# Kernel tuning notes

Hardware: AMD Instinct MI355X
Metric: run time of the kernel (lower is better)

Reference implementation:

```python
import jax, jax.numpy as jnp
import numpy as np

N, E, D = 50000, 600000, 128  # nodes, edges, units (== vert_dim, so no W_adapt)


def glorot(key, shape):
    lim = np.sqrt(6.0 / (shape[0] + shape[1]))
    return jax.random.uniform(key, shape, jnp.float32, -lim, lim)


def setup_inputs() -> dict:
    key = jax.random.key(0)
    ks = jax.random.split(key, 8)
    X = jax.random.normal(ks[0], (N, D), jnp.float32)
    ref_a = jax.random.randint(ks[1], (E,), 0, N, jnp.int32)
    ref_b = jax.random.randint(ks[2], (E,), 0, N, jnp.int32)
    # msg_net: two Dense(D) layers, inner_activation=None (linear)
    W1 = glorot(ks[3], (D, D)); b1 = jnp.zeros((D,), jnp.float32)
    W2 = glorot(ks[4], (D, D)); b2 = jnp.zeros((D,), jnp.float32)
    # keras GRUCell (reset_after=True): kernel [D,3D], recurrent_kernel [D,3D], bias [2,3D]
    gru_kernel = glorot(ks[5], (D, 3 * D))
    gru_rkernel = glorot(ks[6], (D, 3 * D))
    gru_bias = jnp.zeros((2, 3 * D), jnp.float32)
    return {"X": X, "ref_a": ref_a, "ref_b": ref_b,
            "W1": W1, "b1": b1, "W2": W2, "b2": b2,
            "gru_kernel": gru_kernel, "gru_rkernel": gru_rkernel, "gru_bias": gru_bias}


def _ggnn(X, ref_a, ref_b, W1, b1, W2, b2, gru_kernel, gru_rkernel, gru_bias):
    # msg_net (depth=2, linear inner activation)
    X_msg = (X @ W1 + b1) @ W2 + b2                       # [N, D]
    # wl1_convolution, undirected: scatter-add both directions
    agg = jnp.zeros_like(X_msg)
    agg = agg.at[ref_b].add(X_msg[ref_a])                 # a -> b
    agg = agg.at[ref_a].add(X_msg[ref_b])                 # b -> a (directed=False)
    # keras GRUCell update: inputs = agg, state = X  (reset_after=True)
    mx = agg @ gru_kernel + gru_bias[0]                   # [N, 3D]
    mh = X @ gru_rkernel + gru_bias[1]                    # [N, 3D]
    xz, xr, xh = jnp.split(mx, 3, axis=-1)
    rz, rr, rh = jnp.split(mh, 3, axis=-1)
    z = jax.nn.sigmoid(xz + rz)
    r = jax.nn.sigmoid(xr + rr)
    hh = jnp.tanh(xh + r * rh)
    return z * X + (1.0 - z) * hh                         # [N, D]


def reference(X, ref_a, ref_b, W1, b1, W2, b2, gru_kernel, gru_rkernel, gru_bias):
    return _ggnn(X, ref_a, ref_b, W1, b1, W2, b2, gru_kernel, gru_rkernel, gru_bias)
```

## Files before the change

### kernel.cpp

```cpp
#include <hip/hip_runtime.h>
#include <cstdint>
#include <cstddef>

typedef __bf16 bf16x8 __attribute__((ext_vector_type(8)));
typedef float  f32x4  __attribute__((ext_vector_type(4)));
typedef short  s16x8  __attribute__((ext_vector_type(8)));

static __device__ __forceinline__ float bf2f(short s) {
    union { unsigned u; float f; } v;
    v.u = ((unsigned)(unsigned short)s) << 16;
    return v.f;
}
static __device__ __forceinline__ short f2bf(float f) {
    unsigned u = __float_as_uint(f);
    u += 0x7fffu + ((u >> 16) & 1u);
    return (short)(u >> 16);
}
static __device__ __forceinline__ float sigmoid_(float x) {
    return 1.0f / (1.0f + __expf(-x));
}
static __device__ __forceinline__ float tanh_(float x) {
    float ax = fabsf(x);
    float e  = __expf(-2.0f * ax);
    float t  = (1.0f - e) / (1.0f + e);
    return copysignf(t, x);
}

#define MFMA(a, b, c) __builtin_amdgcn_mfma_f32_16x16x32_bf16((a), (b), (c), 0, 0, 0)

static __device__ __forceinline__ int lidx8(int r, int ch) {
    return r * 128 + ((ch ^ (r & 15)) << 3);
}
static __device__ __forceinline__ int lidx(int r, int col) {
    return r * 128 + ((((col >> 3) ^ (r & 15)) << 3) | (col & 7));
}

#define BLOCKS1     256
#define STRIPE_CAP  64
#define BUCKET_REG  (BLOCKS1 * STRIPE_CAP)
#define NODE_CAP    96
#define SENTINEL    0xFFFFFFFFu

__global__ __launch_bounds__(256) void transpose_kernel(
    const float* __restrict__ W1, const float* __restrict__ W2,
    const float* __restrict__ GK, const float* __restrict__ GR,
    short* __restrict__ W1t, short* __restrict__ W2t,
    short* __restrict__ GKt, short* __restrict__ GRt)
{
    int i = blockIdx.x * 256 + threadIdx.x;
    if (i < 16384) {
        int k = i >> 7, n = i & 127;
        W1t[n * 128 + k] = f2bf(W1[i]);
        W2t[n * 128 + k] = f2bf(W2[i]);
    }
    if (i < 49152) {
        int k = i / 384, n = i - k * 384;
        GKt[n * 128 + k] = f2bf(GK[i]);
        GRt[n * 128 + k] = f2bf(GR[i]);
    }
}

static __device__ __forceinline__ s16x8 cvt8(const float* p) {
    f32x4 a0 = *(const f32x4*)(p);
    f32x4 a1 = *(const f32x4*)(p + 4);
    s16x8 v;
    v[0] = f2bf(a0[0]); v[1] = f2bf(a0[1]); v[2] = f2bf(a0[2]); v[3] = f2bf(a0[3]);
    v[4] = f2bf(a1[0]); v[5] = f2bf(a1[1]); v[6] = f2bf(a1[2]); v[7] = f2bf(a1[3]);
    return v;
}

__global__ __launch_bounds__(512) void msg_kernel(
    const float* __restrict__ X, const short* __restrict__ W1t,
    const float* __restrict__ b1, const short* __restrict__ W2t,
    const float* __restrict__ b2, short* __restrict__ msg, int N)
{
    __shared__ short ldsA[128 * 128];
    __shared__ short ldsW[128 * 128];
    const int tid  = threadIdx.x;
    const int m0   = blockIdx.x * 128;
    const int lane = tid & 63, wv = tid >> 6;
    const int q = lane >> 4, c = lane & 15;
    const int rowA0 = wv * 16;

    for (int i = tid; i < 128 * 16; i += 512) {
        int r = i >> 4, ch = i & 15;
        s16x8 v;
        if (m0 + r < N) v = cvt8(X + (size_t)(m0 + r) * 128 + ch * 8);
        else            v = (s16x8)0;
        *(s16x8*)(ldsA + lidx8(r, ch)) = v;
        *(s16x8*)(ldsW + lidx8(r, ch)) = *(const s16x8*)(W1t + r * 128 + ch * 8);
    }
    __syncthreads();

    f32x4 acc[8];
#pragma unroll
    for (int n = 0; n < 8; n++) acc[n] = (f32x4)0.0f;

#pragma unroll
    for (int ks = 0; ks < 4; ks++) {
        int kc = ks * 4 + q;
        bf16x8 a0 = __builtin_bit_cast(bf16x8, *(const s16x8*)(ldsA + lidx8(rowA0 + c, kc)));
#pragma unroll
        for (int n = 0; n < 8; n++) {
            bf16x8 b = __builtin_bit_cast(bf16x8, *(const s16x8*)(ldsW + lidx8(n * 16 + c, kc)));
            acc[n] = MFMA(a0, b, acc[n]);
        }
    }

#pragma unroll
    for (int n = 0; n < 8; n++) {
        float bias = b1[n * 16 + c];
#pragma unroll
        for (int i = 0; i < 4; i++) {
            int row = rowA0 + q * 4 + i;
            ldsA[lidx(row, n * 16 + c)] = f2bf(acc[n][i] + bias);
        }
    }
    __syncthreads();
    for (int i = tid; i < 128 * 16; i += 512) {
        int r = i >> 4, ch = i & 15;
        *(s16x8*)(ldsW + lidx8(r, ch)) = *(const s16x8*)(W2t + r * 128 + ch * 8);
    }
    __syncthreads();

#pragma unroll
    for (int n = 0; n < 8; n++) acc[n] = (f32x4)0.0f;

#pragma unroll
    for (int ks = 0; ks < 4; ks++) {
        int kc = ks * 4 + q;
        bf16x8 a0 = __builtin_bit_cast(bf16x8, *(const s16x8*)(ldsA + lidx8(rowA0 + c, kc)));
#pragma unroll
        for (int n = 0; n < 8; n++) {
            bf16x8 b = __builtin_bit_cast(bf16x8, *(const s16x8*)(ldsW + lidx8(n * 16 + c, kc)));
            acc[n] = MFMA(a0, b, acc[n]);
        }
    }
#pragma unroll
    for (int n = 0; n < 8; n++) {
        float bias = b2[n * 16 + c];
#pragma unroll
        for (int i = 0; i < 4; i++) {
            int row = m0 + rowA0 + q * 4 + i;
            if (row < N) msg[(size_t)row * 128 + n * 16 + c] = f2bf(acc[n][i] + bias);
        }
    }
}

__global__ __launch_bounds__(256) void pass1_kernel(
    const int* __restrict__ ra, const int* __restrict__ rb,
    unsigned* __restrict__ bucketed, int E, int CPB, int nbuckets)
{
    __shared__ int cnt[256];
    cnt[threadIdx.x] = 0;
    __syncthreads();
    const int blk = blockIdx.x;
    const int e1 = min(E, (blk + 1) * CPB);
    for (int e = blk * CPB + threadIdx.x; e < e1; e += 256) {
        int a = ra[e], b = rb[e];
        int ka = a >> 8, kb = b >> 8;
        int r1 = atomicAdd(&cnt[ka], 1);
        if (r1 < STRIPE_CAP)
            bucketed[(size_t)ka * BUCKET_REG + blk * STRIPE_CAP + r1] =
                ((unsigned)(a & 255) << 16) | (unsigned)b;
        int r2 = atomicAdd(&cnt[kb], 1);
        if (r2 < STRIPE_CAP)
            bucketed[(size_t)kb * BUCKET_REG + blk * STRIPE_CAP + r2] =
                ((unsigned)(b & 255) << 16) | (unsigned)a;
    }
    __syncthreads();
    const int total = nbuckets * STRIPE_CAP;
    for (int j = threadIdx.x; j < total; j += 256) {
        int k = j >> 6, slot = j & (STRIPE_CAP - 1);
        if (slot >= min(cnt[k], STRIPE_CAP))
            bucketed[(size_t)k * BUCKET_REG + blk * STRIPE_CAP + slot] = SENTINEL;
    }
}

__global__ __launch_bounds__(256) void pass2_kernel(
    const unsigned* __restrict__ bucketed, unsigned short* __restrict__ nbrS,
    int* __restrict__ counts, int N)
{
    __shared__ int off[256];
    off[threadIdx.x] = 0;
    __syncthreads();
    const int k  = blockIdx.x;
    const int lo = k << 8;
    const unsigned* reg = bucketed + (size_t)k * BUCKET_REG;
    for (int i = threadIdx.x; i < BUCKET_REG; i += 256) {
        unsigned e = reg[i];
        if (e != SENTINEL) {
            int nl = (int)(e >> 16);
            int p  = (int)(e & 0xffffu);
            int r  = atomicAdd(&off[nl], 1);
            if (r < NODE_CAP)
                nbrS[(size_t)(lo + nl) * NODE_CAP + r] = (unsigned short)p;
        }
    }
    __syncthreads();
    int node = lo + threadIdx.x;
    if (node < N) counts[node] = min(off[threadIdx.x], NODE_CAP);
}

__global__ __launch_bounds__(256) void gather_kernel(
    const short* __restrict__ msg, const unsigned short* __restrict__ nbrS,
    const int* __restrict__ counts, short* __restrict__ aggb, int N)
{
    const int lane = threadIdx.x & 63;
    const int node = blockIdx.x * 4 + (threadIdx.x >> 6);
    if (node >= N) return;
    const int g  = lane >> 4;
    const int cl = lane & 15;
    const int s   = node * NODE_CAP;
    const int end = s + counts[node];

    float a[8];
#pragma unroll
    for (int t = 0; t < 8; t++) a[t] = 0.0f;

    int i = s + g;
    for (; i + 12 < end; i += 16) {
        int j0 = (int)nbrS[i];
        int j1 = (int)nbrS[i + 4];
        int j2 = (int)nbrS[i + 8];
        int j3 = (int)nbrS[i + 12];
        s16x8 p0 = *(const s16x8*)(msg + (size_t)j0 * 128 + cl * 8);
        s16x8 p1 = *(const s16x8*)(msg + (size_t)j1 * 128 + cl * 8);
        s16x8 p2 = *(const s16x8*)(msg + (size_t)j2 * 128 + cl * 8);
        s16x8 p3 = *(const s16x8*)(msg + (size_t)j3 * 128 + cl * 8);
#pragma unroll
        for (int t = 0; t < 8; t++) a[t] += bf2f(p0[t]);
#pragma unroll
        for (int t = 0; t < 8; t++) a[t] += bf2f(p1[t]);
#pragma unroll
        for (int t = 0; t < 8; t++) a[t] += bf2f(p2[t]);
#pragma unroll
        for (int t = 0; t < 8; t++) a[t] += bf2f(p3[t]);
    }
    for (; i < end; i += 4) {
        int j = (int)nbrS[i];
        s16x8 p = *(const s16x8*)(msg + (size_t)j * 128 + cl * 8);
#pragma unroll
        for (int t = 0; t < 8; t++) a[t] += bf2f(p[t]);
    }

#pragma unroll
    for (int t = 0; t < 8; t++) {
        a[t] += __shfl_xor(a[t], 32);
        a[t] += __shfl_xor(a[t], 16);
    }
    if (g == 0) {
        s16x8 o;
#pragma unroll
        for (int t = 0; t < 8; t++) o[t] = f2bf(a[t]);
        *(s16x8*)(aggb + (size_t)node * 128 + cl * 8) = o;
    }
}

__global__ __launch_bounds__(512) void gru_kernel(
    const short* __restrict__ aggb, const float* __restrict__ X,
    const short* __restrict__ GKt, const short* __restrict__ GRt,
    const float* __restrict__ gbias, float* __restrict__ out, int N)
{
    __shared__ short ldsA[128 * 128];
    __shared__ short ldsX[128 * 128];
    const int tid  = threadIdx.x;
    const int m0   = blockIdx.x * 128;
    const int lane = tid & 63, wv = tid >> 6;
    const int q = lane >> 4, c = lane & 15;

    for (int i = tid; i < 128 * 16; i += 512) {
        int r = i >> 4, ch = i & 15;
        s16x8 vx, va;
        if (m0 + r < N) {
            vx = cvt8(X + (size_t)(m0 + r) * 128 + ch * 8);
            va = *(const s16x8*)(aggb + (size_t)(m0 + r) * 128 + ch * 8);
        } else { vx = (s16x8)0; va = (s16x8)0; }
        *(s16x8*)(ldsX + lidx8(r, ch)) = vx;
        *(s16x8*)(ldsA + lidx8(r, ch)) = va;
    }
    __syncthreads();

    const int nt   = wv;
    const int ncol = nt * 16 + c;

    bf16x8 bkz[4], bkr[4], bkh[4], brz[4], brr[4], brh[4];
#pragma unroll
    for (int ks = 0; ks < 4; ks++) {
        int ko = ks * 32 + q * 8;
        bkz[ks] = __builtin_bit_cast(bf16x8, *(const s16x8*)(GKt + (size_t)(ncol)       * 128 + ko));
        bkr[ks] = __builtin_bit_cast(bf16x8, *(const s16x8*)(GKt + (size_t)(128 + ncol) * 128 + ko));
        bkh[ks] = __builtin_bit_cast(bf16x8, *(const s16x8*)(GKt + (size_t)(256 + ncol) * 128 + ko));
        brz[ks] = __builtin_bit_cast(bf16x8, *(const s16x8*)(GRt + (size_t)(ncol)       * 128 + ko));
        brr[ks] = __builtin_bit_cast(bf16x8, *(const s16x8*)(GRt + (size_t)(128 + ncol) * 128 + ko));
        brh[ks] = __builtin_bit_cast(bf16x8, *(const s16x8*)(GRt + (size_t)(256 + ncol) * 128 + ko));
    }
    float bz0 = gbias[ncol],       br0 = gbias[128 + ncol],       bh0 = gbias[256 + ncol];
    float bz1 = gbias[384 + ncol], br1 = gbias[384 + 128 + ncol], bh1 = gbias[384 + 256 + ncol];

#pragma clang loop unroll(disable)
    for (int rt = 0; rt < 8; rt++) {
        float xv[4];
#pragma unroll
        for (int i = 0; i < 4; i++) {
            int grow = m0 + rt * 16 + q * 4 + i;
            xv[i] = (grow < N) ? X[(size_t)grow * 128 + ncol] : 0.0f;
        }
        f32x4 axz = (f32x4)0.0f, axr = (f32x4)0.0f, axh = (f32x4)0.0f;
        f32x4 arz = (f32x4)0.0f, arr = (f32x4)0.0f, arh = (f32x4)0.0f;
#pragma unroll
        for (int ks = 0; ks < 4; ks++) {
            int kc = ks * 4 + q;
            bf16x8 aA = __builtin_bit_cast(bf16x8, *(const s16x8*)(ldsA + lidx8(rt * 16 + c, kc)));
            bf16x8 aX = __builtin_bit_cast(bf16x8, *(const s16x8*)(ldsX + lidx8(rt * 16 + c, kc)));
            axz = MFMA(aA, bkz[ks], axz);
            axr = MFMA(aA, bkr[ks], axr);
            axh = MFMA(aA, bkh[ks], axh);
            arz = MFMA(aX, brz[ks], arz);
            arr = MFMA(aX, brr[ks], arr);
            arh = MFMA(aX, brh[ks], arh);
        }
#pragma unroll
        for (int i = 0; i < 4; i++) {
            int grow = m0 + rt * 16 + q * 4 + i;
            if (grow < N) {
                float z  = sigmoid_(axz[i] + bz0 + arz[i] + bz1);
                float r  = sigmoid_(axr[i] + br0 + arr[i] + br1);
                float hh = tanh_(axh[i] + bh0 + r * (arh[i] + bh1));
                out[(size_t)grow * 128 + ncol] = z * xv[i] + (1.0f - z) * hh;
            }
        }
    }
}

extern "C" void kernel_launch(void* const* d_in, const int* in_sizes, int n_in,
                              void* d_out, int out_size, void* d_ws, size_t ws_size,
                              hipStream_t stream)
{
    const float* X  = (const float*)d_in[0];
    const int*   ra = (const int*)d_in[1];
    const int*   rb = (const int*)d_in[2];
    const float* W1 = (const float*)d_in[3];
    const float* b1 = (const float*)d_in[4];
    const float* W2 = (const float*)d_in[5];
    const float* b2 = (const float*)d_in[6];
    const float* GK = (const float*)d_in[7];
    const float* GR = (const float*)d_in[8];
    const float* GB = (const float*)d_in[9];
    const int N = in_sizes[0] / 128;
    const int E = in_sizes[1];
    float* out = (float*)d_out;

    const int nbuckets = (N + 255) >> 8;

    char* ws = (char*)d_ws;
    size_t off = 0;
    short* aggb   = (short*)(ws + off);   off += (size_t)N * 128 * 2;
    short* msg    = (short*)(ws + off);   off += (size_t)N * 128 * 2;
    short* W1t    = (short*)(ws + off);   off += 16384u * 2;
    short* W2t    = (short*)(ws + off);   off += 16384u * 2;
    short* GKt    = (short*)(ws + off);   off += 49152u * 2;
    short* GRt    = (short*)(ws + off);   off += 49152u * 2;
    unsigned* bucketed = (unsigned*)(ws + off);
    off += (size_t)nbuckets * BUCKET_REG * 4;
    unsigned short* nbrS = (unsigned short*)(ws + off);
    off += (size_t)nbuckets * 256 * NODE_CAP * 2;
    int* counts   = (int*)(ws + off);     off += (size_t)N * 4;

    transpose_kernel<<<192, 256, 0, stream>>>(W1, W2, GK, GR, W1t, W2t, GKt, GRt);

    const int CPB = (E + BLOCKS1 - 1) / BLOCKS1;
    pass1_kernel<<<BLOCKS1, 256, 0, stream>>>(ra, rb, bucketed, E, CPB, nbuckets);
    pass2_kernel<<<nbuckets, 256, 0, stream>>>(bucketed, nbrS, counts, N);

    const int nblk = (N + 127) / 128;
    msg_kernel<<<nblk, 512, 0, stream>>>(X, W1t, b1, W2t, b2, msg, N);
    gather_kernel<<<(N + 3) / 4, 256, 0, stream>>>(msg, nbrS, counts, aggb, N);
    gru_kernel<<<nblk, 512, 0, stream>>>(aggb, X, GKt, GRt, GB, out, N);
}
```

Baseline: 222.1 us.

## Merge weight transpose into edge bucketing and co-launch msg GEMM with pass2

Folds the weight transpose/convert into the edge-bucketing kernel, and merges the message MLP with the second bucketing pass into one launch whose trailing blocks handle pass2. This cuts the launch count from six to four and lets independent work overlap. The message and GRU kernels now use 64-row tiles with weights held in registers per wave, which halves LDS use and doubles the block count for better occupancy. The cost is more redundant per-block weight loads and heterogeneous blocks within one grid.

After: 203.6 us. -8.3%, faster.

```diff
diff --git a/kernel.cpp b/kernel.cpp
--- a/kernel.cpp
+++ b/kernel.cpp
@@ -40,25 +40,6 @@
 #define BUCKET_REG  (BLOCKS1 * STRIPE_CAP)
 #define NODE_CAP    96
 #define SENTINEL    0xFFFFFFFFu
-
-__global__ __launch_bounds__(256) void transpose_kernel(
-    const float* __restrict__ W1, const float* __restrict__ W2,
-    const float* __restrict__ GK, const float* __restrict__ GR,
-    short* __restrict__ W1t, short* __restrict__ W2t,
-    short* __restrict__ GKt, short* __restrict__ GRt)
-{
-    int i = blockIdx.x * 256 + threadIdx.x;
-    if (i < 16384) {
-        int k = i >> 7, n = i & 127;
-        W1t[n * 128 + k] = f2bf(W1[i]);
-        W2t[n * 128 + k] = f2bf(W2[i]);
-    }
-    if (i < 49152) {
-        int k = i / 384, n = i - k * 384;
-        GKt[n * 128 + k] = f2bf(GK[i]);
-        GRt[n * 128 + k] = f2bf(GR[i]);
-    }
-}
 
 static __device__ __forceinline__ s16x8 cvt8(const float* p) {
     f32x4 a0 = *(const f32x4*)(p);
@@ -69,91 +50,30 @@
     return v;
 }
 
-__global__ __launch_bounds__(512) void msg_kernel(
-    const float* __restrict__ X, const short* __restrict__ W1t,
-    const float* __restrict__ b1, const short* __restrict__ W2t,
-    const float* __restrict__ b2, short* __restrict__ msg, int N)
-{
-    __shared__ short ldsA[128 * 128];
-    __shared__ short ldsW[128 * 128];
-    const int tid  = threadIdx.x;
-    const int m0   = blockIdx.x * 128;
-    const int lane = tid & 63, wv = tid >> 6;
-    const int q = lane >> 4, c = lane & 15;
-    const int rowA0 = wv * 16;
-
-    for (int i = tid; i < 128 * 16; i += 512) {
-        int r = i >> 4, ch = i & 15;
-        s16x8 v;
-        if (m0 + r < N) v = cvt8(X + (size_t)(m0 + r) * 128 + ch * 8);
-        else            v = (s16x8)0;
-        *(s16x8*)(ldsA + lidx8(r, ch)) = v;
-        *(s16x8*)(ldsW + lidx8(r, ch)) = *(const s16x8*)(W1t + r * 128 + ch * 8);
-    }
-    __syncthreads();
-
-    f32x4 acc[8];
-#pragma unroll
-    for (int n = 0; n < 8; n++) acc[n] = (f32x4)0.0f;
-
-#pragma unroll
-    for (int ks = 0; ks < 4; ks++) {
-        int kc = ks * 4 + q;
-        bf16x8 a0 = __builtin_bit_cast(bf16x8, *(const s16x8*)(ldsA + lidx8(rowA0 + c, kc)));
-#pragma unroll
-        for (int n = 0; n < 8; n++) {
-            bf16x8 b = __builtin_bit_cast(bf16x8, *(const s16x8*)(ldsW + lidx8(n * 16 + c, kc)));
-            acc[n] = MFMA(a0, b, acc[n]);
-        }
-    }
-
-#pragma unroll
-    for (int n = 0; n < 8; n++) {
-        float bias = b1[n * 16 + c];
-#pragma unroll
-        for (int i = 0; i < 4; i++) {
-            int row = rowA0 + q * 4 + i;
-            ldsA[lidx(row, n * 16 + c)] = f2bf(acc[n][i] + bias);
-        }
-    }
-    __syncthreads();
-    for (int i = tid; i < 128 * 16; i += 512) {
-        int r = i >> 4, ch = i & 15;
-        *(s16x8*)(ldsW + lidx8(r, ch)) = *(const s16x8*)(W2t + r * 128 + ch * 8);
-    }
-    __syncthreads();
-
-#pragma unroll
-    for (int n = 0; n < 8; n++) acc[n] = (f32x4)0.0f;
-
-#pragma unroll
-    for (int ks = 0; ks < 4; ks++) {
-        int kc = ks * 4 + q;
-        bf16x8 a0 = __builtin_bit_cast(bf16x8, *(const s16x8*)(ldsA + lidx8(rowA0 + c, kc)));
-#pragma unroll
-        for (int n = 0; n < 8; n++) {
-            bf16x8 b = __builtin_bit_cast(bf16x8, *(const s16x8*)(ldsW + lidx8(n * 16 + c, kc)));
-            acc[n] = MFMA(a0, b, acc[n]);
-        }
-    }
-#pragma unroll
-    for (int n = 0; n < 8; n++) {
-        float bias = b2[n * 16 + c];
-#pragma unroll
-        for (int i = 0; i < 4; i++) {
-            int row = m0 + rowA0 + q * 4 + i;
-            if (row < N) msg[(size_t)row * 128 + n * 16 + c] = f2bf(acc[n][i] + bias);
-        }
-    }
-}
-
-__global__ __launch_bounds__(256) void pass1_kernel(
+__global__ __launch_bounds__(256) void prep_kernel(
     const int* __restrict__ ra, const int* __restrict__ rb,
-    unsigned* __restrict__ bucketed, int E, int CPB, int nbuckets)
+    unsigned* __restrict__ bucketed, int E, int CPB, int nbuckets,
+    const float* __restrict__ W1, const float* __restrict__ W2,
+    const float* __restrict__ GK, const float* __restrict__ GR,
+    short* __restrict__ W1t, short* __restrict__ W2t,
+    short* __restrict__ GKt, short* __restrict__ GRt)
 {
     __shared__ int cnt[256];
     cnt[threadIdx.x] = 0;
-    __syncthreads();
+
+    int i = blockIdx.x * 256 + threadIdx.x;
+    if (i < 16384) {
+        int k = i >> 7, n = i & 127;
+        W1t[n * 128 + k] = f2bf(W1[i]);
+        W2t[n * 128 + k] = f2bf(W2[i]);
+    }
+    if (i < 49152) {
+        int k = i / 384, n = i - k * 384;
+        GKt[n * 128 + k] = f2bf(GK[i]);
+        GRt[n * 128 + k] = f2bf(GR[i]);
+    }
+    __syncthreads();
+
     const int blk = blockIdx.x;
     const int e1 = min(E, (blk + 1) * CPB);
     for (int e = blk * CPB + threadIdx.x; e < e1; e += 256) {
@@ -177,29 +97,101 @@
     }
 }
 
-__global__ __launch_bounds__(256) void pass2_kernel(
+__global__ __launch_bounds__(512) void msg_pass2_kernel(
+    const float* __restrict__ X, const short* __restrict__ W1t,
+    const float* __restrict__ b1, const short* __restrict__ W2t,
+    const float* __restrict__ b2, short* __restrict__ msg, int N, int nblk64,
     const unsigned* __restrict__ bucketed, unsigned short* __restrict__ nbrS,
-    int* __restrict__ counts, int N)
-{
+    int* __restrict__ counts)
+{
+    __shared__ short ldsA[64 * 128];
+    __shared__ short ldsY[64 * 128];
     __shared__ int off[256];
-    off[threadIdx.x] = 0;
-    __syncthreads();
-    const int k  = blockIdx.x;
-    const int lo = k << 8;
-    const unsigned* reg = bucketed + (size_t)k * BUCKET_REG;
-    for (int i = threadIdx.x; i < BUCKET_REG; i += 256) {
-        unsigned e = reg[i];
-        if (e != SENTINEL) {
-            int nl = (int)(e >> 16);
-            int p  = (int)(e & 0xffffu);
-            int r  = atomicAdd(&off[nl], 1);
-            if (r < NODE_CAP)
-                nbrS[(size_t)(lo + nl) * NODE_CAP + r] = (unsigned short)p;
-        }
-    }
-    __syncthreads();
-    int node = lo + threadIdx.x;
-    if (node < N) counts[node] = min(off[threadIdx.x], NODE_CAP);
+    const int tid = threadIdx.x;
+
+    if ((int)blockIdx.x >= nblk64) {
+        const int k = blockIdx.x - nblk64;
+        if (tid < 256) off[tid] = 0;
+        __syncthreads();
+        const int lo = k << 8;
+        const unsigned* reg = bucketed + (size_t)k * BUCKET_REG;
+        for (int i = tid; i < BUCKET_REG; i += 512) {
+            unsigned e = reg[i];
+            if (e != SENTINEL) {
+                int nl = (int)(e >> 16);
+                int p  = (int)(e & 0xffffu);
+                int r  = atomicAdd(&off[nl], 1);
+                if (r < NODE_CAP)
+                    nbrS[(size_t)(lo + nl) * NODE_CAP + r] = (unsigned short)p;
+            }
+        }
+        __syncthreads();
+        int node = lo + tid;
+        if (tid < 256 && node < N) counts[node] = min(off[tid], NODE_CAP);
+        return;
+    }
+
+    const int m0   = blockIdx.x * 64;
+    const int lane = tid & 63, wv = tid >> 6;
+    const int q = lane >> 4, c = lane & 15;
+    const int ncol = wv * 16 + c;
+
+    bf16x8 w1f[4], w2f[4];
+#pragma unroll
+    for (int ks = 0; ks < 4; ks++) {
+        int ko = ks * 32 + q * 8;
+        w1f[ks] = __builtin_bit_cast(bf16x8, *(const s16x8*)(W1t + (size_t)ncol * 128 + ko));
+        w2f[ks] = __builtin_bit_cast(bf16x8, *(const s16x8*)(W2t + (size_t)ncol * 128 + ko));
+    }
+
+    for (int i = tid; i < 64 * 16; i += 512) {
+        int r = i >> 4, ch = i & 15;
+        s16x8 v;
+        if (m0 + r < N) v = cvt8(X + (size_t)(m0 + r) * 128 + ch * 8);
+        else            v = (s16x8)0;
+        *(s16x8*)(ldsA + lidx8(r, ch)) = v;
+    }
+    __syncthreads();
+
+    f32x4 acc[4];
+#pragma unroll
+    for (int rt = 0; rt < 4; rt++) acc[rt] = (f32x4)0.0f;
+#pragma unroll
+    for (int ks = 0; ks < 4; ks++) {
+        int kc = ks * 4 + q;
+#pragma unroll
+        for (int rt = 0; rt < 4; rt++) {
+            bf16x8 aA = __builtin_bit_cast(bf16x8, *(const s16x8*)(ldsA + lidx8(rt * 16 + c, kc)));
+            acc[rt] = MFMA(aA, w1f[ks], acc[rt]);
+        }
+    }
+    float bias1 = b1[ncol];
+#pragma unroll
+    for (int rt = 0; rt < 4; rt++)
+#pragma unroll
+        for (int i = 0; i < 4; i++)
+            ldsY[lidx(rt * 16 + q * 4 + i, ncol)] = f2bf(acc[rt][i] + bias1);
+    __syncthreads();
+
+#pragma unroll
+    for (int rt = 0; rt < 4; rt++) acc[rt] = (f32x4)0.0f;
+#pragma unroll
+    for (int ks = 0; ks < 4; ks++) {
+        int kc = ks * 4 + q;
+#pragma unroll
+        for (int rt = 0; rt < 4; rt++) {
+            bf16x8 aY = __builtin_bit_cast(bf16x8, *(const s16x8*)(ldsY + lidx8(rt * 16 + c, kc)));
+            acc[rt] = MFMA(aY, w2f[ks], acc[rt]);
+        }
+    }
+    float bias2 = b2[ncol];
+#pragma unroll
+    for (int rt = 0; rt < 4; rt++)
+#pragma unroll
+        for (int i = 0; i < 4; i++) {
+            int row = m0 + rt * 16 + q * 4 + i;
+            if (row < N) msg[(size_t)row * 128 + ncol] = f2bf(acc[rt][i] + bias2);
+        }
 }
 
 __global__ __launch_bounds__(256) void gather_kernel(
@@ -262,14 +254,29 @@
     const short* __restrict__ GKt, const short* __restrict__ GRt,
     const float* __restrict__ gbias, float* __restrict__ out, int N)
 {
-    __shared__ short ldsA[128 * 128];
-    __shared__ short ldsX[128 * 128];
+    __shared__ short ldsA[64 * 128];
+    __shared__ short ldsX[64 * 128];
     const int tid  = threadIdx.x;
-    const int m0   = blockIdx.x * 128;
+    const int m0   = blockIdx.x * 64;
     const int lane = tid & 63, wv = tid >> 6;
     const int q = lane >> 4, c = lane & 15;
-
-    for (int i = tid; i < 128 * 16; i += 512) {
+    const int ncol = wv * 16 + c;
+
+    bf16x8 bkz[4], bkr[4], bkh[4], brz[4], brr[4], brh[4];
+#pragma unroll
+    for (int ks = 0; ks < 4; ks++) {
+        int ko = ks * 32 + q * 8;
+        bkz[ks] = __builtin_bit_cast(bf16x8, *(const s16x8*)(GKt + (size_t)(ncol)       * 128 + ko));
+        bkr[ks] = __builtin_bit_cast(bf16x8, *(const s16x8*)(GKt + (size_t)(128 + ncol) * 128 + ko));
+        bkh[ks] = __builtin_bit_cast(bf16x8, *(const s16x8*)(GKt + (size_t)(256 + ncol) * 128 + ko));
+        brz[ks] = __builtin_bit_cast(bf16x8, *(const s16x8*)(GRt + (size_t)(ncol)       * 128 + ko));
+        brr[ks] = __builtin_bit_cast(bf16x8, *(const s16x8*)(GRt + (size_t)(128 + ncol) * 128 + ko));
+        brh[ks] = __builtin_bit_cast(bf16x8, *(const s16x8*)(GRt + (size_t)(256 + ncol) * 128 + ko));
+    }
+    float bz0 = gbias[ncol],       br0 = gbias[128 + ncol],       bh0 = gbias[256 + ncol];
+    float bz1 = gbias[384 + ncol], br1 = gbias[384 + 128 + ncol], bh1 = gbias[384 + 256 + ncol];
+
+    for (int i = tid; i < 64 * 16; i += 512) {
         int r = i >> 4, ch = i & 15;
         s16x8 vx, va;
         if (m0 + r < N) {
@@ -281,25 +288,8 @@
     }
     __syncthreads();
 
-    const int nt   = wv;
-    const int ncol = nt * 16 + c;
-
-    bf16x8 bkz[4], bkr[4], bkh[4], brz[4], brr[4], brh[4];
-#pragma unroll
-    for (int ks = 0; ks < 4; ks++) {
-        int ko = ks * 32 + q * 8;
-        bkz[ks] = __builtin_bit_cast(bf16x8, *(const s16x8*)(GKt + (size_t)(ncol)       * 128 + ko));
-        bkr[ks] = __builtin_bit_cast(bf16x8, *(const s16x8*)(GKt + (size_t)(128 + ncol) * 128 + ko));
-        bkh[ks] = __builtin_bit_cast(bf16x8, *(const s16x8*)(GKt + (size_t)(256 + ncol) * 128 + ko));
-        brz[ks] = __builtin_bit_cast(bf16x8, *(const s16x8*)(GRt + (size_t)(ncol)       * 128 + ko));
-        brr[ks] = __builtin_bit_cast(bf16x8, *(const s16x8*)(GRt + (size_t)(128 + ncol) * 128 + ko));
-        brh[ks] = __builtin_bit_cast(bf16x8, *(const s16x8*)(GRt + (size_t)(256 + ncol) * 128 + ko));
-    }
-    float bz0 = gbias[ncol],       br0 = gbias[128 + ncol],       bh0 = gbias[256 + ncol];
-    float bz1 = gbias[384 + ncol], br1 = gbias[384 + 128 + ncol], bh1 = gbias[384 + 256 + ncol];
-
 #pragma clang loop unroll(disable)
-    for (int rt = 0; rt < 8; rt++) {
+    for (int rt = 0; rt < 4; rt++) {
         float xv[4];
 #pragma unroll
         for (int i = 0; i < 4; i++) {
@@ -367,14 +357,14 @@
     off += (size_t)nbuckets * 256 * NODE_CAP * 2;
     int* counts   = (int*)(ws + off);     off += (size_t)N * 4;
 
-    transpose_kernel<<<192, 256, 0, stream>>>(W1, W2, GK, GR, W1t, W2t, GKt, GRt);
-
     const int CPB = (E + BLOCKS1 - 1) / BLOCKS1;
-    pass1_kernel<<<BLOCKS1, 256, 0, stream>>>(ra, rb, bucketed, E, CPB, nbuckets);
-    pass2_kernel<<<nbuckets, 256, 0, stream>>>(bucketed, nbrS, counts, N);
-
-    const int nblk = (N + 127) / 128;
-    msg_kernel<<<nblk, 512, 0, stream>>>(X, W1t, b1, W2t, b2, msg, N);
+    prep_kernel<<<BLOCKS1, 256, 0, stream>>>(ra, rb, bucketed, E, CPB, nbuckets,
+                                             W1, W2, GK, GR, W1t, W2t, GKt, GRt);
+
+    const int nblk64 = (N + 63) / 64;
+    msg_pass2_kernel<<<nblk64 + nbuckets, 512, 0, stream>>>(
+        X, W1t, b1, W2t, b2, msg, N, nblk64, bucketed, nbrS, counts);
+
     gather_kernel<<<(N + 3) / 4, 256, 0, stream>>>(msg, nbrS, counts, aggb, N);
-    gru_kernel<<<nblk, 512, 0, stream>>>(aggb, X, GKt, GRt, GB, out, N);
-}
+    gru_kernel<<<nblk64, 512, 0, stream>>>(aggb, X, GKt, GRt, GB, out, N);
+}
```
